# Performance work log

Hardware: AMD Instinct MI355X
Metric: run time of the kernel (lower is better)

## Reference

```python
import jax, jax.numpy as jnp
import numpy as np

NUM_QUERIES = 300


def setup_inputs() -> dict:
    key = jax.random.key(0)
    k1, k2, k3 = jax.random.split(key, 3)
    d_model = 256
    tokens = jax.random.normal(k1, (16, 20000, d_model), dtype=jnp.float32)
    # nn.Linear(d_model, 1): weight [1, d_model], bias [1]; store as vector/scalar
    W = jax.random.normal(k2, (d_model,), dtype=jnp.float32) / np.sqrt(d_model)
    b = jax.random.normal(k3, (), dtype=jnp.float32) * 0.01
    return {"tokens": tokens, "W": W, "b": b}


def reference(tokens, W, b):
    # scores: [B, N] -- scalar linear projection per token
    scores = jnp.einsum("bnd,d->bn", tokens, W) + b
    k = min(NUM_QUERIES, tokens.shape[1])
    _, topk = jax.lax.top_k(scores, k)  # [B, k], sorted by descending score
    # gather full token vectors at selected indices: [B, k, d]
    selected = jnp.take_along_axis(tokens, topk[..., None], axis=1)
    return selected, topk
```

## Files before the change

### kernel.cpp

```cpp
#include <hip/hip_runtime.h>
#include <stdint.h>

#define B 16
#define N 20000
#define D 256
#define K 300

__global__ __launch_bounds__(256) void score_kernel(
    const float* __restrict__ tokens, const float* __restrict__ W,
    const float* __restrict__ bias, uint32_t* __restrict__ keys) {
  int wid = (blockIdx.x * blockDim.x + threadIdx.x) >> 6;
  int lane = threadIdx.x & 63;
  int tb = wid * 4;
  if (tb >= B * N) return;
  const float4 w4 = ((const float4*)W)[lane];
  const float4* tp = (const float4*)(tokens + (size_t)tb * D);
  float4 a0 = tp[lane];
  float4 a1 = tp[64 + lane];
  float4 a2 = tp[128 + lane];
  float4 a3 = tp[192 + lane];
  float d0 = a0.x * w4.x + a0.y * w4.y + a0.z * w4.z + a0.w * w4.w;
  float d1 = a1.x * w4.x + a1.y * w4.y + a1.z * w4.z + a1.w * w4.w;
  float d2 = a2.x * w4.x + a2.y * w4.y + a2.z * w4.z + a2.w * w4.w;
  float d3 = a3.x * w4.x + a3.y * w4.y + a3.z * w4.z + a3.w * w4.w;
#pragma unroll
  for (int off = 32; off >= 1; off >>= 1) {
    d0 += __shfl_xor(d0, off, 64);
    d1 += __shfl_xor(d1, off, 64);
    d2 += __shfl_xor(d2, off, 64);
    d3 += __shfl_xor(d3, off, 64);
  }
  if (lane == 0) {
    float bb = bias[0];
    float s0 = d0 + bb, s1 = d1 + bb, s2 = d2 + bb, s3 = d3 + bb;
    uint32_t u0 = __float_as_uint(s0), u1 = __float_as_uint(s1);
    uint32_t u2 = __float_as_uint(s2), u3 = __float_as_uint(s3);
    uint4 kv;
    kv.x = (u0 & 0x80000000u) ? ~u0 : (u0 | 0x80000000u);
    kv.y = (u1 & 0x80000000u) ? ~u1 : (u1 | 0x80000000u);
    kv.z = (u2 & 0x80000000u) ? ~u2 : (u2 | 0x80000000u);
    kv.w = (u3 & 0x80000000u) ? ~u3 : (u3 | 0x80000000u);
    ((uint4*)keys)[wid] = kv;
  }
}

__global__ __launch_bounds__(1024) void topk_kernel(
    const uint32_t* __restrict__ keys_g, int* __restrict__ idx_out,
    float* __restrict__ out_idx_f) {
  __shared__ __align__(16) uint32_t hist[256];
  __shared__ uint64_t cand[512];
  __shared__ uint32_t s_prefix, s_remaining, s_prefix_next, s_rem_next,
      cand_cnt;

  const int b = blockIdx.x;
  const int t = threadIdx.x;
  const uint4* keys4 = (const uint4*)(keys_g + (size_t)b * N);
  const int N4 = N / 4;

  if (t == 0) {
    s_prefix = 0;
    s_remaining = K;
    cand_cnt = 0;
  }
  if (t < 256) hist[t] = 0;
  __syncthreads();

  for (int pass = 0; pass < 4; ++pass) {
    const int shift = 24 - pass * 8;
    const uint32_t prefix = s_prefix;
    const uint32_t pmask = (pass == 0) ? 0u : (0xFFFFFFFFu << (shift + 8));
    for (int i = t; i < N4; i += 1024) {
      uint4 kv = keys4[i];
      uint32_t ka[4] = {kv.x, kv.y, kv.z, kv.w};
#pragma unroll
      for (int j = 0; j < 4; ++j)
        if ((ka[j] & pmask) == prefix)
          atomicAdd(&hist[(ka[j] >> shift) & 255u], 1u);
    }
    __syncthreads();
    if (t < 64) {
      uint4 h = ((const uint4*)hist)[t];
      uint32_t hv0 = h.x, hv1 = h.y, hv2 = h.z, hv3 = h.w;
      uint32_t sum4 = hv0 + hv1 + hv2 + hv3;
      uint32_t s = sum4;
#pragma unroll
      for (int off = 1; off < 64; off <<= 1) {
        uint32_t v = __shfl_down(s, off, 64);
        if (t + off < 64) s += v;
      }
      uint32_t rem = s_remaining;
      uint32_t acc = s - sum4;
      uint32_t hv[4] = {hv0, hv1, hv2, hv3};
#pragma unroll
      for (int j = 3; j >= 0; --j) {
        uint32_t ge = acc + hv[j];
        if (acc < rem && rem <= ge) {
          s_prefix_next = prefix | ((uint32_t)(4 * t + j) << shift);
          s_rem_next = rem - acc;
        }
        acc = ge;
      }
    }
    __syncthreads();
    if (t == 0) {
      s_prefix = s_prefix_next;
      s_remaining = s_rem_next;
    }
    if (t < 256) hist[t] = 0;
    __syncthreads();
  }
  const uint32_t T = s_prefix;

  for (int i = t; i < N4; i += 1024) {
    uint4 kv = keys4[i];
    uint32_t ka[4] = {kv.x, kv.y, kv.z, kv.w};
#pragma unroll
    for (int j = 0; j < 4; ++j)
      if (ka[j] >= T) {
        uint32_t pos = atomicAdd(&cand_cnt, 1u);
        if (pos < 512)
          cand[pos] = ((uint64_t)ka[j] << 32) |
                      (uint64_t)(0xFFFFFFFFu - (uint32_t)(4 * i + j));
      }
  }
  __syncthreads();
  int cnt = (int)cand_cnt;
  if (cnt > 512) cnt = 512;
  if (t < 512 && t >= cnt) cand[t] = 0;
  __syncthreads();

  for (int ksz = 2; ksz <= 512; ksz <<= 1) {
    for (int j = ksz >> 1; j >= 1; j >>= 1) {
      if (t < 512) {
        int ixj = t ^ j;
        if (ixj > t) {
          uint64_t a = cand[t], c = cand[ixj];
          bool desc = ((t & ksz) == 0);
          if (desc ? (a < c) : (a > c)) {
            cand[t] = c;
            cand[ixj] = a;
          }
        }
      }
      __syncthreads();
    }
  }

  if (t < K) {
    int idx = (int)(0xFFFFFFFFu - (uint32_t)(cand[t] & 0xFFFFFFFFu));
    idx_out[b * K + t] = idx;
    out_idx_f[b * K + t] = (float)idx;
  }
}

__global__ __launch_bounds__(256) void gather_kernel(
    const float* __restrict__ tokens, const int* __restrict__ idx,
    float* __restrict__ out0) {
  int gwave = (blockIdx.x * blockDim.x + threadIdx.x) >> 6;
  int lane = threadIdx.x & 63;
  if (gwave >= B * K) return;
  int b = gwave / K;
  int id = idx[gwave];
  float4 v = ((const float4*)(tokens + ((size_t)b * N + id) * D))[lane];
  ((float4*)(out0 + (size_t)gwave * D))[lane] = v;
}

extern "C" void kernel_launch(void* const* d_in, const int* in_sizes, int n_in,
                              void* d_out, int out_size, void* d_ws,
                              size_t ws_size, hipStream_t stream) {
  const float* tokens = (const float*)d_in[0];
  const float* W = (const float*)d_in[1];
  const float* bias = (const float*)d_in[2];

  float* out_sel = (float*)d_out;
  float* out_idx_f = out_sel + (size_t)B * K * D;

  uint32_t* keys = (uint32_t*)d_ws;
  int* idx = (int*)((char*)d_ws + (size_t)B * N * sizeof(uint32_t));

  score_kernel<<<(B * N) / 16, 256, 0, stream>>>(tokens, W, bias, keys);
  topk_kernel<<<B, 1024, 0, stream>>>(keys, idx, out_idx_f);
  gather_kernel<<<(B * K + 3) / 4, 256, 0, stream>>>(tokens, idx, out_sel);
}
```

Measured before the change: 448.7 us.

## Batch score reductions, aggregate histogram atomics, replace bitonic sort with rank sort

Result: slower. 497.8 us (+10.9%).

```diff
diff --git a/kernel.cpp b/kernel.cpp
--- a/kernel.cpp
+++ b/kernel.cpp
@@ -11,40 +11,49 @@
     const float* __restrict__ bias, uint32_t* __restrict__ keys) {
   int wid = (blockIdx.x * blockDim.x + threadIdx.x) >> 6;
   int lane = threadIdx.x & 63;
-  int tb = wid * 4;
+  int tb = wid * 8;
   if (tb >= B * N) return;
   const float4 w4 = ((const float4*)W)[lane];
   const float4* tp = (const float4*)(tokens + (size_t)tb * D);
-  float4 a0 = tp[lane];
-  float4 a1 = tp[64 + lane];
-  float4 a2 = tp[128 + lane];
-  float4 a3 = tp[192 + lane];
-  float d0 = a0.x * w4.x + a0.y * w4.y + a0.z * w4.z + a0.w * w4.w;
-  float d1 = a1.x * w4.x + a1.y * w4.y + a1.z * w4.z + a1.w * w4.w;
-  float d2 = a2.x * w4.x + a2.y * w4.y + a2.z * w4.z + a2.w * w4.w;
-  float d3 = a3.x * w4.x + a3.y * w4.y + a3.z * w4.z + a3.w * w4.w;
+  float d[8];
 #pragma unroll
-  for (int off = 32; off >= 1; off >>= 1) {
-    d0 += __shfl_xor(d0, off, 64);
-    d1 += __shfl_xor(d1, off, 64);
-    d2 += __shfl_xor(d2, off, 64);
-    d3 += __shfl_xor(d3, off, 64);
+  for (int j = 0; j < 8; ++j) {
+    float4 a = tp[j * 64 + lane];
+    d[j] = a.x * w4.x + a.y * w4.y + a.z * w4.z + a.w * w4.w;
   }
-  if (lane == 0) {
-    float bb = bias[0];
-    float s0 = d0 + bb, s1 = d1 + bb, s2 = d2 + bb, s3 = d3 + bb;
-    uint32_t u0 = __float_as_uint(s0), u1 = __float_as_uint(s1);
-    uint32_t u2 = __float_as_uint(s2), u3 = __float_as_uint(s3);
-    uint4 kv;
-    kv.x = (u0 & 0x80000000u) ? ~u0 : (u0 | 0x80000000u);
-    kv.y = (u1 & 0x80000000u) ? ~u1 : (u1 | 0x80000000u);
-    kv.z = (u2 & 0x80000000u) ? ~u2 : (u2 | 0x80000000u);
-    kv.w = (u3 & 0x80000000u) ? ~u3 : (u3 | 0x80000000u);
-    ((uint4*)keys)[wid] = kv;
+  float m0, m1, m2, m3, s, r;
+  s = (lane & 1) ? d[0] : d[1];
+  r = __shfl_xor(s, 1, 64);
+  m0 = ((lane & 1) ? d[1] : d[0]) + r;
+  s = (lane & 1) ? d[2] : d[3];
+  r = __shfl_xor(s, 1, 64);
+  m1 = ((lane & 1) ? d[3] : d[2]) + r;
+  s = (lane & 1) ? d[4] : d[5];
+  r = __shfl_xor(s, 1, 64);
+  m2 = ((lane & 1) ? d[5] : d[4]) + r;
+  s = (lane & 1) ? d[6] : d[7];
+  r = __shfl_xor(s, 1, 64);
+  m3 = ((lane & 1) ? d[7] : d[6]) + r;
+  float e0, e1;
+  s = (lane & 2) ? m0 : m1;
+  r = __shfl_xor(s, 2, 64);
+  e0 = ((lane & 2) ? m1 : m0) + r;
+  s = (lane & 2) ? m2 : m3;
+  r = __shfl_xor(s, 2, 64);
+  e1 = ((lane & 2) ? m3 : m2) + r;
+  s = (lane & 4) ? e0 : e1;
+  r = __shfl_xor(s, 4, 64);
+  float f = ((lane & 4) ? e1 : e0) + r;
+  f += __shfl_xor(f, 8, 64);
+  f += __shfl_xor(f, 16, 64);
+  f += __shfl_xor(f, 32, 64);
+  if (lane < 8) {
+    uint32_t u = __float_as_uint(f + bias[0]);
+    keys[tb + lane] = (u & 0x80000000u) ? ~u : (u | 0x80000000u);
   }
 }
 
-__global__ __launch_bounds__(1024) void topk_kernel(
+__global__ __launch_bounds__(512) void topk_kernel(
     const uint32_t* __restrict__ keys_g, int* __restrict__ idx_out,
     float* __restrict__ out_idx_f) {
   __shared__ __align__(16) uint32_t hist[256];
@@ -54,6 +63,7 @@
 
   const int b = blockIdx.x;
   const int t = threadIdx.x;
+  const int lane = t & 63;
   const uint4* keys4 = (const uint4*)(keys_g + (size_t)b * N);
   const int N4 = N / 4;
 
@@ -69,13 +79,24 @@
     const int shift = 24 - pass * 8;
     const uint32_t prefix = s_prefix;
     const uint32_t pmask = (pass == 0) ? 0u : (0xFFFFFFFFu << (shift + 8));
-    for (int i = t; i < N4; i += 1024) {
-      uint4 kv = keys4[i];
+    for (int i = t; i < 5120; i += 512) {
+      const bool in = i < N4;
+      uint4 kv;
+      if (in) kv = keys4[i];
       uint32_t ka[4] = {kv.x, kv.y, kv.z, kv.w};
 #pragma unroll
-      for (int j = 0; j < 4; ++j)
-        if ((ka[j] & pmask) == prefix)
-          atomicAdd(&hist[(ka[j] >> shift) & 255u], 1u);
+      for (int j = 0; j < 4; ++j) {
+        const bool p = in && ((ka[j] & pmask) == prefix);
+        const uint32_t bin = (ka[j] >> shift) & 255u;
+        unsigned long long todo = __ballot(p);
+        while (todo) {
+          const int leader = __ffsll(todo) - 1;
+          const uint32_t lbin = __shfl(bin, leader, 64);
+          const unsigned long long same = __ballot(p && (bin == lbin));
+          if (lane == leader) atomicAdd(&hist[lbin], (uint32_t)__popcll(same));
+          todo &= ~same;
+        }
+      }
     }
     __syncthreads();
     if (t < 64) {
@@ -111,45 +132,33 @@
   }
   const uint32_t T = s_prefix;
 
-  for (int i = t; i < N4; i += 1024) {
-    uint4 kv = keys4[i];
-    uint32_t ka[4] = {kv.x, kv.y, kv.z, kv.w};
+  for (int i = t; i < 5120; i += 512) {
+    if (i < N4) {
+      uint4 kv = keys4[i];
+      uint32_t ka[4] = {kv.x, kv.y, kv.z, kv.w};
 #pragma unroll
-    for (int j = 0; j < 4; ++j)
-      if (ka[j] >= T) {
-        uint32_t pos = atomicAdd(&cand_cnt, 1u);
-        if (pos < 512)
-          cand[pos] = ((uint64_t)ka[j] << 32) |
-                      (uint64_t)(0xFFFFFFFFu - (uint32_t)(4 * i + j));
-      }
+      for (int j = 0; j < 4; ++j)
+        if (ka[j] >= T) {
+          uint32_t pos = atomicAdd(&cand_cnt, 1u);
+          if (pos < 512)
+            cand[pos] = ((uint64_t)ka[j] << 32) |
+                        (uint64_t)(0xFFFFFFFFu - (uint32_t)(4 * i + j));
+        }
+    }
   }
   __syncthreads();
+
   int cnt = (int)cand_cnt;
   if (cnt > 512) cnt = 512;
-  if (t < 512 && t >= cnt) cand[t] = 0;
-  __syncthreads();
-
-  for (int ksz = 2; ksz <= 512; ksz <<= 1) {
-    for (int j = ksz >> 1; j >= 1; j >>= 1) {
-      if (t < 512) {
-        int ixj = t ^ j;
-        if (ixj > t) {
-          uint64_t a = cand[t], c = cand[ixj];
-          bool desc = ((t & ksz) == 0);
-          if (desc ? (a < c) : (a > c)) {
-            cand[t] = c;
-            cand[ixj] = a;
-          }
-        }
-      }
-      __syncthreads();
+  if (t < cnt) {
+    const uint64_t mine = cand[t];
+    int rank = 0;
+    for (int i = 0; i < cnt; ++i) rank += (cand[i] > mine) ? 1 : 0;
+    if (rank < K) {
+      int idx = (int)(0xFFFFFFFFu - (uint32_t)(mine & 0xFFFFFFFFu));
+      idx_out[b * K + rank] = idx;
+      out_idx_f[b * K + rank] = (float)idx;
     }
-  }
-
-  if (t < K) {
-    int idx = (int)(0xFFFFFFFFu - (uint32_t)(cand[t] & 0xFFFFFFFFu));
-    idx_out[b * K + t] = idx;
-    out_idx_f[b * K + t] = (float)idx;
   }
 }
 
@@ -178,7 +187,7 @@
   uint32_t* keys = (uint32_t*)d_ws;
   int* idx = (int*)((char*)d_ws + (size_t)B * N * sizeof(uint32_t));
 
-  score_kernel<<<(B * N) / 16, 256, 0, stream>>>(tokens, W, bias, keys);
-  topk_kernel<<<B, 1024, 0, stream>>>(keys, idx, out_idx_f);
+  score_kernel<<<(B * N) / 32, 256, 0, stream>>>(tokens, W, bias, keys);
+  topk_kernel<<<B, 512, 0, stream>>>(keys, idx, out_idx_f);
   gather_kernel<<<(B * K + 3) / 4, 256, 0, stream>>>(tokens, idx, out_sel);
 }
```
